# Optimization experiments

Hardware: AMD Instinct MI355X
Metric: run time of the kernel (lower is better)

## Reference

```python
import jax, jax.numpy as jnp
import numpy as np

INITIAL_CAPITAL = 500.0
TRANSACTION_COST = 0.0003
TAU = 1.0  # gumbel-softmax temperature
B, S, F = 256, 4096, 64


def setup_inputs() -> dict:
    key = jax.random.key(0)
    ks = jax.random.split(key, 10)
    features = jax.random.normal(ks[0], (B, S, F), dtype=jnp.float32)
    # make columns 1/2 look like vix level / vix change so branches fire
    features = features.at[:, :, 1].set(20.0 + 10.0 * jax.random.uniform(ks[1], (B, S)))
    features = features.at[:, :, 2].set(0.5 * jax.random.normal(ks[2], (B, S)))
    features = features.at[:, :, 3].set(0.01 * jax.random.normal(ks[3], (B, S)))
    return {
        "features": features,
        "feature_weights": jnp.ones((F,), jnp.float32) / F,
        "long_threshold": jnp.float32(0.52),
        "short_threshold": jnp.float32(0.48),
        "base_position_size": jnp.float32(0.8),
        "conviction_scalar": jnp.float32(0.5),
        "vix_impact": jnp.float32(0.2),
        "vix_collapse_threshold": jnp.float32(0.15),
        "vix_spike_threshold": jnp.float32(0.15),
        "gumbel_noise": jax.random.gumbel(ks[4], (S, B, 3), dtype=jnp.float32),
    }


def reference(features, feature_weights, long_threshold, short_threshold,
              base_position_size, conviction_scalar, vix_impact,
              vix_collapse_threshold, vix_spike_threshold, gumbel_noise):
    batch, seq_len, _ = features.shape
    # predictions: sigmoid of feature-weighted sum  [B,S]
    predictions = jax.nn.sigmoid(jnp.einsum('bsf,f->bs', features, feature_weights))
    # time-major per-step inputs [S,B]
    pred_t = predictions.T
    mom_t = features[:, :, 0].T
    vix_t = features[:, :, 1].T
    vch_t = features[:, :, 2].T
    mret_t = features[:, :, 3].T

    def step(carry, x):
        eq, pos = carry  # eq [B], pos [B,3]
        p, v, dv, m, r, g = x
        signal_strength = jnp.abs(p - 0.5) / 0.5
        vix_collapse = (dv < -vix_collapse_threshold) & (v < 30.0)
        vix_spike = (dv > vix_spike_threshold) & (v > 20.0)
        psz = jnp.clip(base_position_size + conviction_scalar * signal_strength, 0.2, 1.0)
        psz = jnp.where(vix_collapse | vix_spike, psz * (1.0 + vix_impact), psz)
        long_pos = ((p >= long_threshold) & (m > 0)) | vix_collapse
        short_pos = ((p <= short_threshold) & (m < 0)) | vix_spike
        logits = jnp.stack([
            jnp.where(long_pos, 1.0, -10.0),
            jnp.where(short_pos, 1.0, -10.0),
            jnp.where(~long_pos & ~short_pos, 1.0, -10.0),
        ], axis=1)  # [B,3]
        probs = jax.nn.softmax((logits + g) / TAU, axis=1)
        strategy_return = psz * (probs[:, 0] - probs[:, 1]) * r
        position_change = jnp.abs(probs - pos).sum(axis=1)
        eq_new = eq * (1.0 + strategy_return - position_change * TRANSACTION_COST)
        return (eq_new, probs), (eq_new, probs, psz)

    eq0 = jnp.full((batch,), INITIAL_CAPITAL, dtype=features.dtype)
    pos0 = jnp.zeros((batch, 3), features.dtype).at[:, 2].set(1.0)
    (_, _), (eq_seq, pos_seq, psz_seq) = jax.lax.scan(
        step, (eq0, pos0), (pred_t, vix_t, vch_t, mom_t, mret_t, gumbel_noise))
    equity = jnp.concatenate([eq0[:, None], eq_seq.T], axis=1)          # [B,S+1]
    positions = jnp.concatenate([pos0[:, None], jnp.swapaxes(pos_seq, 0, 1)], axis=1)  # [B,S+1,3]
    position_sizes = psz_seq[-1]  # last timestep, matching torch loop leak
    return equity, positions, predictions, position_sizes
```

## Files before the change

### kernel.cpp

```cpp
#include <hip/hip_runtime.h>

#define Bn 256
#define Sn 4096
#define Fn 64
#define TCOST 0.0003f
#define INIT_CAP 500.0f

#define EQ_OFF   0
#define POS_OFF  (Bn * (Sn + 1))
#define PRED_OFF (Bn * (Sn + 1) * 4)
#define PSZ_OFF  (PRED_OFF + Bn * Sn)

__global__ __launch_bounds__(256) void gumbel_transpose(
    const float* __restrict__ gin,
    float* __restrict__ gout)
{
    __shared__ float tile[32 * 97];
    int s0 = (blockIdx.x & 127) * 32;
    int b0 = (blockIdx.x >> 7) * 32;

    for (int idx = threadIdx.x; idx < 32 * 96; idx += 256) {
        int i = idx / 96;
        int rem = idx - i * 96;
        tile[i * 97 + rem] = gin[(size_t)(s0 + i) * (Bn * 3) + b0 * 3 + rem];
    }
    __syncthreads();
    for (int idx = threadIdx.x; idx < 32 * 96; idx += 256) {
        int j = idx / 96;
        int rem = idx - j * 96;
        int i = rem / 3;
        int c = rem - i * 3;
        gout[(size_t)(b0 + j) * (Sn * 3) + (size_t)(s0 + i) * 3 + c] =
            tile[i * 97 + j * 3 + c];
    }
}

__global__ __launch_bounds__(256) void trishot_fwd(
    const float* __restrict__ feat,
    const float* __restrict__ w,
    const float* __restrict__ p_lt, const float* __restrict__ p_st,
    const float* __restrict__ p_bps, const float* __restrict__ p_cs,
    const float* __restrict__ p_vi, const float* __restrict__ p_vct,
    const float* __restrict__ p_vst,
    const float* __restrict__ gt,
    float* __restrict__ out)
{
    __shared__ float xs[256];
    __shared__ float m0s[256], v0s[256], d0s[256], r0s[256];

    int t = threadIdx.x;
    int R0 = blockIdx.x * 256;
    int g = t >> 4;
    int l = t & 15;

    float4 wv = ((const float4*)w)[l];

#pragma unroll
    for (int q = 0; q < 16; q++) {
        int row = R0 + q * 16 + g;
        float4 fv = ((const float4*)feat)[(size_t)row * 16 + l];
        float partial = fmaf(fv.x, wv.x,
                        fmaf(fv.y, wv.y,
                        fmaf(fv.z, wv.z, fv.w * wv.w)));
        partial += __shfl_xor(partial, 1, 64);
        partial += __shfl_xor(partial, 2, 64);
        partial += __shfl_xor(partial, 4, 64);
        partial += __shfl_xor(partial, 8, 64);
        if (l == 0) {
            int rr = q * 16 + g;
            xs[rr]  = partial;
            m0s[rr] = fv.x;
            v0s[rr] = fv.y;
            d0s[rr] = fv.z;
            r0s[rr] = fv.w;
        }
    }
    __syncthreads();

    int r = R0 + t;
    int b = r >> 12;
    int s = r & (Sn - 1);

    const float LT = *p_lt, ST = *p_st, BPS = *p_bps, CS = *p_cs,
                VI = *p_vi, VCT = *p_vct, VST = *p_vst;

    float x = xs[t];
    float p = 1.0f / (1.0f + __expf(-x));
    float mom = m0s[t], vix = v0s[t], dvix = d0s[t], mret = r0s[t];

    float ss = fabsf(p - 0.5f) * 2.0f;
    bool collapse = (dvix < -VCT) && (vix < 30.0f);
    bool spike    = (dvix >  VST) && (vix > 20.0f);
    float psz = fminf(fmaxf(BPS + CS * ss, 0.2f), 1.0f);
    if (collapse || spike) psz *= (1.0f + VI);

    bool lp = ((p >= LT) && (mom > 0.0f)) || collapse;
    bool sp = ((p <= ST) && (mom < 0.0f)) || spike;
    float l0 = lp ? 1.0f : -10.0f;
    float l1 = sp ? 1.0f : -10.0f;
    float l2 = (!lp && !sp) ? 1.0f : -10.0f;

    const float* gg = gt + (size_t)r * 3;
    float g0 = gg[0], g1 = gg[1], g2 = gg[2];
    float z0 = l0 + g0, z1 = l1 + g1, z2 = l2 + g2;
    float zm = fmaxf(z0, fmaxf(z1, z2));
    float e0 = __expf(z0 - zm), e1 = __expf(z1 - zm), e2 = __expf(z2 - zm);
    float inv = 1.0f / (e0 + e1 + e2);
    float q0 = e0 * inv, q1 = e1 * inv, q2 = e2 * inv;

    out[PRED_OFF + r] = p;

    size_t prow = ((size_t)b * (Sn + 1) + s + 1) * 3;
    float* pos = out + POS_OFF;
    pos[prow + 0] = q0;
    pos[prow + 1] = q1;
    pos[prow + 2] = q2;

    out[EQ_OFF + (size_t)b * (Sn + 1) + s + 1] = psz * (q0 - q1) * mret;

    if (s == 0) {
        size_t p0row = (size_t)b * (Sn + 1) * 3;
        pos[p0row + 0] = 0.0f;
        pos[p0row + 1] = 0.0f;
        pos[p0row + 2] = 1.0f;
    }
    if (s == Sn - 1) {
        out[PSZ_OFF + b] = psz;
    }
}

#define CH 16
__global__ __launch_bounds__(256) void trishot_scan(float* __restrict__ out)
{
    int b = blockIdx.x;
    int j = threadIdx.x;

    float* eq = out + EQ_OFF + (size_t)b * (Sn + 1);
    const float* pos = out + POS_OFF + (size_t)b * (Sn + 1) * 3;

    int t0 = j * CH;
    float prev0 = pos[(size_t)t0 * 3 + 0];
    float prev1 = pos[(size_t)t0 * 3 + 1];
    float prev2 = pos[(size_t)t0 * 3 + 2];

    float f[CH];
    float lprod = 1.0f;
#pragma unroll
    for (int i = 0; i < CH; i++) {
        size_t ci = (size_t)(t0 + i + 1) * 3;
        float c0 = pos[ci + 0], c1 = pos[ci + 1], c2 = pos[ci + 2];
        float pc = fabsf(c0 - prev0) + fabsf(c1 - prev1) + fabsf(c2 - prev2);
        float rp = eq[t0 + i + 1];
        float fac = 1.0f + rp - pc * TCOST;
        f[i] = fac;
        lprod *= fac;
        prev0 = c0; prev1 = c1; prev2 = c2;
    }

    __shared__ float sc[256];
    sc[j] = lprod;
    __syncthreads();
#pragma unroll
    for (int off = 1; off < 256; off <<= 1) {
        float mine = sc[j];
        float other = (j >= off) ? sc[j - off] : 1.0f;
        __syncthreads();
        sc[j] = mine * other;
        __syncthreads();
    }

    float eqv = INIT_CAP * ((j > 0) ? sc[j - 1] : 1.0f);
#pragma unroll
    for (int i = 0; i < CH; i++) {
        eqv *= f[i];
        eq[t0 + i + 1] = eqv;
    }
    if (j == 0) eq[0] = INIT_CAP;
}

extern "C" void kernel_launch(void* const* d_in, const int* in_sizes, int n_in,
                              void* d_out, int out_size, void* d_ws, size_t ws_size,
                              hipStream_t stream) {
    const float* feat   = (const float*)d_in[0];
    const float* w      = (const float*)d_in[1];
    const float* lt     = (const float*)d_in[2];
    const float* st     = (const float*)d_in[3];
    const float* bps    = (const float*)d_in[4];
    const float* cs     = (const float*)d_in[5];
    const float* vi     = (const float*)d_in[6];
    const float* vct    = (const float*)d_in[7];
    const float* vst    = (const float*)d_in[8];
    const float* gumbel = (const float*)d_in[9];
    float* out = (float*)d_out;
    float* gt  = (float*)d_ws;

    gumbel_transpose<<<128 * 8, 256, 0, stream>>>(gumbel, gt);
    trishot_fwd<<<(Bn * Sn) / 256, 256, 0, stream>>>(
        feat, w, lt, st, bps, cs, vi, vct, vst, gt, out);
    trishot_scan<<<Bn, 256, 0, stream>>>(out);
}
```

Before: 402.1 us.

## Fuse forward pass and equity scan into one block-per-batch kernel

Merges the per-row forward kernel and the equity scan kernel into a single kernel with one 1024-thread block per batch row. Softmax positions and per-step factors stay in shared memory, so the scan no longer re-reads positions and returns from global memory, and one launch is dropped. In exchange, grid parallelism falls to one block per batch, shared memory use grows, and chunked processing adds block-wide barriers, which can reduce latency hiding for the large feature read.

After: 396.6 us. About the same (-1.4%).

```diff
diff --git a/kernel.cpp b/kernel.cpp
--- a/kernel.cpp
+++ b/kernel.cpp
@@ -35,7 +35,7 @@
     }
 }
 
-__global__ __launch_bounds__(256) void trishot_fwd(
+__global__ __launch_bounds__(1024) void trishot_fused(
     const float* __restrict__ feat,
     const float* __restrict__ w,
     const float* __restrict__ p_lt, const float* __restrict__ p_st,
@@ -45,137 +45,123 @@
     const float* __restrict__ gt,
     float* __restrict__ out)
 {
-    __shared__ float xs[256];
-    __shared__ float m0s[256], v0s[256], d0s[256], r0s[256];
+    __shared__ float qL[(Sn + 1) * 3];
+    __shared__ float facL[Sn];
+    __shared__ float xs[1024];
+    __shared__ float m0s[1024], v0s[1024], d0s[1024], r0s[1024];
+    __shared__ float scanL[1024];
 
+    int b = blockIdx.x;
     int t = threadIdx.x;
-    int R0 = blockIdx.x * 256;
     int g = t >> 4;
     int l = t & 15;
-
-    float4 wv = ((const float4*)w)[l];
-
-#pragma unroll
-    for (int q = 0; q < 16; q++) {
-        int row = R0 + q * 16 + g;
-        float4 fv = ((const float4*)feat)[(size_t)row * 16 + l];
-        float partial = fmaf(fv.x, wv.x,
-                        fmaf(fv.y, wv.y,
-                        fmaf(fv.z, wv.z, fv.w * wv.w)));
-        partial += __shfl_xor(partial, 1, 64);
-        partial += __shfl_xor(partial, 2, 64);
-        partial += __shfl_xor(partial, 4, 64);
-        partial += __shfl_xor(partial, 8, 64);
-        if (l == 0) {
-            int rr = q * 16 + g;
-            xs[rr]  = partial;
-            m0s[rr] = fv.x;
-            v0s[rr] = fv.y;
-            d0s[rr] = fv.z;
-            r0s[rr] = fv.w;
-        }
-    }
-    __syncthreads();
-
-    int r = R0 + t;
-    int b = r >> 12;
-    int s = r & (Sn - 1);
 
     const float LT = *p_lt, ST = *p_st, BPS = *p_bps, CS = *p_cs,
                 VI = *p_vi, VCT = *p_vct, VST = *p_vst;
 
-    float x = xs[t];
-    float p = 1.0f / (1.0f + __expf(-x));
-    float mom = m0s[t], vix = v0s[t], dvix = d0s[t], mret = r0s[t];
+    float4 wv = ((const float4*)w)[l];
 
-    float ss = fabsf(p - 0.5f) * 2.0f;
-    bool collapse = (dvix < -VCT) && (vix < 30.0f);
-    bool spike    = (dvix >  VST) && (vix > 20.0f);
-    float psz = fminf(fmaxf(BPS + CS * ss, 0.2f), 1.0f);
-    if (collapse || spike) psz *= (1.0f + VI);
+    if (t == 0) { qL[0] = 0.0f; qL[1] = 0.0f; qL[2] = 1.0f; }
 
-    bool lp = ((p >= LT) && (mom > 0.0f)) || collapse;
-    bool sp = ((p <= ST) && (mom < 0.0f)) || spike;
-    float l0 = lp ? 1.0f : -10.0f;
-    float l1 = sp ? 1.0f : -10.0f;
-    float l2 = (!lp && !sp) ? 1.0f : -10.0f;
+    float* pos = out + POS_OFF;
 
-    const float* gg = gt + (size_t)r * 3;
-    float g0 = gg[0], g1 = gg[1], g2 = gg[2];
-    float z0 = l0 + g0, z1 = l1 + g1, z2 = l2 + g2;
-    float zm = fmaxf(z0, fmaxf(z1, z2));
-    float e0 = __expf(z0 - zm), e1 = __expf(z1 - zm), e2 = __expf(z2 - zm);
-    float inv = 1.0f / (e0 + e1 + e2);
-    float q0 = e0 * inv, q1 = e1 * inv, q2 = e2 * inv;
+    for (int c = 0; c < 4; c++) {
+#pragma unroll
+        for (int q = 0; q < 16; q++) {
+            int i = q * 64 + g;
+            size_t row = (size_t)b * Sn + c * 1024 + i;
+            float4 fv = ((const float4*)feat)[row * 16 + l];
+            float partial = fmaf(fv.x, wv.x,
+                            fmaf(fv.y, wv.y,
+                            fmaf(fv.z, wv.z, fv.w * wv.w)));
+            partial += __shfl_xor(partial, 1, 64);
+            partial += __shfl_xor(partial, 2, 64);
+            partial += __shfl_xor(partial, 4, 64);
+            partial += __shfl_xor(partial, 8, 64);
+            if (l == 0) {
+                xs[i]  = partial;
+                m0s[i] = fv.x;
+                v0s[i] = fv.y;
+                d0s[i] = fv.z;
+                r0s[i] = fv.w;
+            }
+        }
+        __syncthreads();
 
-    out[PRED_OFF + r] = p;
+        int s = c * 1024 + t;
+        float x = xs[t];
+        float p = 1.0f / (1.0f + __expf(-x));
+        float mom = m0s[t], vix = v0s[t], dvix = d0s[t], mret = r0s[t];
 
-    size_t prow = ((size_t)b * (Sn + 1) + s + 1) * 3;
-    float* pos = out + POS_OFF;
-    pos[prow + 0] = q0;
-    pos[prow + 1] = q1;
-    pos[prow + 2] = q2;
+        float ss = fabsf(p - 0.5f) * 2.0f;
+        bool collapse = (dvix < -VCT) && (vix < 30.0f);
+        bool spike    = (dvix >  VST) && (vix > 20.0f);
+        float psz = fminf(fmaxf(BPS + CS * ss, 0.2f), 1.0f);
+        if (collapse || spike) psz *= (1.0f + VI);
 
-    out[EQ_OFF + (size_t)b * (Sn + 1) + s + 1] = psz * (q0 - q1) * mret;
+        bool lp = ((p >= LT) && (mom > 0.0f)) || collapse;
+        bool sp = ((p <= ST) && (mom < 0.0f)) || spike;
+        float l0 = lp ? 1.0f : -10.0f;
+        float l1 = sp ? 1.0f : -10.0f;
+        float l2 = (!lp && !sp) ? 1.0f : -10.0f;
 
-    if (s == 0) {
+        const float* gg = gt + ((size_t)b * Sn + s) * 3;
+        float z0 = l0 + gg[0], z1 = l1 + gg[1], z2 = l2 + gg[2];
+        float zm = fmaxf(z0, fmaxf(z1, z2));
+        float e0 = __expf(z0 - zm), e1 = __expf(z1 - zm), e2 = __expf(z2 - zm);
+        float inv = 1.0f / (e0 + e1 + e2);
+        float q0 = e0 * inv, q1 = e1 * inv, q2 = e2 * inv;
+
+        qL[(s + 1) * 3 + 0] = q0;
+        qL[(s + 1) * 3 + 1] = q1;
+        qL[(s + 1) * 3 + 2] = q2;
+
+        out[PRED_OFF + (size_t)b * Sn + s] = p;
+        size_t prow = ((size_t)b * (Sn + 1) + s + 1) * 3;
+        pos[prow + 0] = q0;
+        pos[prow + 1] = q1;
+        pos[prow + 2] = q2;
+        if (s == Sn - 1) out[PSZ_OFF + b] = psz;
+
+        float rp = psz * (q0 - q1) * mret;
+        __syncthreads();
+
+        float pm0 = qL[s * 3 + 0], pm1 = qL[s * 3 + 1], pm2 = qL[s * 3 + 2];
+        float pc = fabsf(q0 - pm0) + fabsf(q1 - pm1) + fabsf(q2 - pm2);
+        facL[s] = 1.0f + rp - pc * TCOST;
+        __syncthreads();
+    }
+
+    float f0 = facL[4 * t + 0];
+    float f1 = facL[4 * t + 1];
+    float f2 = facL[4 * t + 2];
+    float f3 = facL[4 * t + 3];
+    float lprod = ((f0 * f1) * (f2 * f3));
+    scanL[t] = lprod;
+    __syncthreads();
+#pragma unroll
+    for (int off = 1; off < 1024; off <<= 1) {
+        float mine = scanL[t];
+        float other = (t >= off) ? scanL[t - off] : 1.0f;
+        __syncthreads();
+        scanL[t] = mine * other;
+        __syncthreads();
+    }
+
+    float* eq = out + EQ_OFF + (size_t)b * (Sn + 1);
+    float eqv = INIT_CAP * ((t > 0) ? scanL[t - 1] : 1.0f);
+    eqv *= f0; eq[4 * t + 1] = eqv;
+    eqv *= f1; eq[4 * t + 2] = eqv;
+    eqv *= f2; eq[4 * t + 3] = eqv;
+    eqv *= f3; eq[4 * t + 4] = eqv;
+
+    if (t == 0) {
+        eq[0] = INIT_CAP;
         size_t p0row = (size_t)b * (Sn + 1) * 3;
         pos[p0row + 0] = 0.0f;
         pos[p0row + 1] = 0.0f;
         pos[p0row + 2] = 1.0f;
     }
-    if (s == Sn - 1) {
-        out[PSZ_OFF + b] = psz;
-    }
-}
-
-#define CH 16
-__global__ __launch_bounds__(256) void trishot_scan(float* __restrict__ out)
-{
-    int b = blockIdx.x;
-    int j = threadIdx.x;
-
-    float* eq = out + EQ_OFF + (size_t)b * (Sn + 1);
-    const float* pos = out + POS_OFF + (size_t)b * (Sn + 1) * 3;
-
-    int t0 = j * CH;
-    float prev0 = pos[(size_t)t0 * 3 + 0];
-    float prev1 = pos[(size_t)t0 * 3 + 1];
-    float prev2 = pos[(size_t)t0 * 3 + 2];
-
-    float f[CH];
-    float lprod = 1.0f;
-#pragma unroll
-    for (int i = 0; i < CH; i++) {
-        size_t ci = (size_t)(t0 + i + 1) * 3;
-        float c0 = pos[ci + 0], c1 = pos[ci + 1], c2 = pos[ci + 2];
-        float pc = fabsf(c0 - prev0) + fabsf(c1 - prev1) + fabsf(c2 - prev2);
-        float rp = eq[t0 + i + 1];
-        float fac = 1.0f + rp - pc * TCOST;
-        f[i] = fac;
-        lprod *= fac;
-        prev0 = c0; prev1 = c1; prev2 = c2;
-    }
-
-    __shared__ float sc[256];
-    sc[j] = lprod;
-    __syncthreads();
-#pragma unroll
-    for (int off = 1; off < 256; off <<= 1) {
-        float mine = sc[j];
-        float other = (j >= off) ? sc[j - off] : 1.0f;
-        __syncthreads();
-        sc[j] = mine * other;
-        __syncthreads();
-    }
-
-    float eqv = INIT_CAP * ((j > 0) ? sc[j - 1] : 1.0f);
-#pragma unroll
-    for (int i = 0; i < CH; i++) {
-        eqv *= f[i];
-        eq[t0 + i + 1] = eqv;
-    }
-    if (j == 0) eq[0] = INIT_CAP;
 }
 
 extern "C" void kernel_launch(void* const* d_in, const int* in_sizes, int n_in,
@@ -195,7 +181,6 @@
     float* gt  = (float*)d_ws;
 
     gumbel_transpose<<<128 * 8, 256, 0, stream>>>(gumbel, gt);
-    trishot_fwd<<<(Bn * Sn) / 256, 256, 0, stream>>>(
+    trishot_fused<<<Bn, 1024, 0, stream>>>(
         feat, w, lt, st, bps, cs, vi, vct, vst, gt, out);
-    trishot_scan<<<Bn, 256, 0, stream>>>(out);
 }
```

## Compute per-step equity factor in forward kernel, drop position reads in scan

Applied to the files above, without the earlier changes.

The forward kernel now keeps each block's softmax probabilities in shared memory and also computes the previous row's probabilities for the block boundary. With those it computes the full per-step growth factor (1 + return - transaction cost) directly. The scan kernel then reads only that factor and no longer re-reads the positions array from global memory. This removes about 3 floats per step of global reads in the scan, at the cost of a small redundant boundary-row computation and an extra barrier per block.

After: 402.6 us. Within noise of the previous version (+0.1%).

```diff
diff --git a/kernel.cpp b/kernel.cpp
--- a/kernel.cpp
+++ b/kernel.cpp
@@ -47,13 +47,52 @@
 {
     __shared__ float xs[256];
     __shared__ float m0s[256], v0s[256], d0s[256], r0s[256];
+    __shared__ float qs[257 * 3];
 
     int t = threadIdx.x;
     int R0 = blockIdx.x * 256;
     int g = t >> 4;
     int l = t & 15;
 
+    const float LT = *p_lt, ST = *p_st, BPS = *p_bps, CS = *p_cs,
+                VI = *p_vi, VCT = *p_vct, VST = *p_vst;
+
     float4 wv = ((const float4*)w)[l];
+
+    int s0 = R0 & (Sn - 1);
+    int b = R0 >> 12;
+
+    if (t < 16) {
+        if (s0 == 0) {
+            if (t == 0) { qs[0] = 0.0f; qs[1] = 0.0f; qs[2] = 1.0f; }
+        } else {
+            float4 fv = ((const float4*)feat)[(size_t)(R0 - 1) * 16 + t];
+            float partial = fmaf(fv.x, wv.x,
+                            fmaf(fv.y, wv.y,
+                            fmaf(fv.z, wv.z, fv.w * wv.w)));
+            partial += __shfl_xor(partial, 1, 64);
+            partial += __shfl_xor(partial, 2, 64);
+            partial += __shfl_xor(partial, 4, 64);
+            partial += __shfl_xor(partial, 8, 64);
+            if (t == 0) {
+                float p = 1.0f / (1.0f + __expf(-partial));
+                float mom = fv.x, vix = fv.y, dvix = fv.z;
+                bool collapse = (dvix < -VCT) && (vix < 30.0f);
+                bool spike    = (dvix >  VST) && (vix > 20.0f);
+                bool lp = ((p >= LT) && (mom > 0.0f)) || collapse;
+                bool sp = ((p <= ST) && (mom < 0.0f)) || spike;
+                float l0 = lp ? 1.0f : -10.0f;
+                float l1 = sp ? 1.0f : -10.0f;
+                float l2 = (!lp && !sp) ? 1.0f : -10.0f;
+                const float* gg = gt + (size_t)(R0 - 1) * 3;
+                float z0 = l0 + gg[0], z1 = l1 + gg[1], z2 = l2 + gg[2];
+                float zm = fmaxf(z0, fmaxf(z1, z2));
+                float e0 = __expf(z0 - zm), e1 = __expf(z1 - zm), e2 = __expf(z2 - zm);
+                float inv = 1.0f / (e0 + e1 + e2);
+                qs[0] = e0 * inv; qs[1] = e1 * inv; qs[2] = e2 * inv;
+            }
+        }
+    }
 
 #pragma unroll
     for (int q = 0; q < 16; q++) {
@@ -77,13 +116,7 @@
     }
     __syncthreads();
 
-    int r = R0 + t;
-    int b = r >> 12;
-    int s = r & (Sn - 1);
-
-    const float LT = *p_lt, ST = *p_st, BPS = *p_bps, CS = *p_cs,
-                VI = *p_vi, VCT = *p_vct, VST = *p_vst;
-
+    int s = s0 + t;
     float x = xs[t];
     float p = 1.0f / (1.0f + __expf(-x));
     float mom = m0s[t], vix = v0s[t], dvix = d0s[t], mret = r0s[t];
@@ -100,33 +133,37 @@
     float l1 = sp ? 1.0f : -10.0f;
     float l2 = (!lp && !sp) ? 1.0f : -10.0f;
 
-    const float* gg = gt + (size_t)r * 3;
-    float g0 = gg[0], g1 = gg[1], g2 = gg[2];
-    float z0 = l0 + g0, z1 = l1 + g1, z2 = l2 + g2;
+    const float* gg = gt + (size_t)(R0 + t) * 3;
+    float z0 = l0 + gg[0], z1 = l1 + gg[1], z2 = l2 + gg[2];
     float zm = fmaxf(z0, fmaxf(z1, z2));
     float e0 = __expf(z0 - zm), e1 = __expf(z1 - zm), e2 = __expf(z2 - zm);
     float inv = 1.0f / (e0 + e1 + e2);
     float q0 = e0 * inv, q1 = e1 * inv, q2 = e2 * inv;
 
-    out[PRED_OFF + r] = p;
-
+    qs[(t + 1) * 3 + 0] = q0;
+    qs[(t + 1) * 3 + 1] = q1;
+    qs[(t + 1) * 3 + 2] = q2;
+
+    out[PRED_OFF + R0 + t] = p;
+    float* pos = out + POS_OFF;
     size_t prow = ((size_t)b * (Sn + 1) + s + 1) * 3;
-    float* pos = out + POS_OFF;
     pos[prow + 0] = q0;
     pos[prow + 1] = q1;
     pos[prow + 2] = q2;
-
-    out[EQ_OFF + (size_t)b * (Sn + 1) + s + 1] = psz * (q0 - q1) * mret;
-
+    if (s == Sn - 1) out[PSZ_OFF + b] = psz;
     if (s == 0) {
         size_t p0row = (size_t)b * (Sn + 1) * 3;
         pos[p0row + 0] = 0.0f;
         pos[p0row + 1] = 0.0f;
         pos[p0row + 2] = 1.0f;
     }
-    if (s == Sn - 1) {
-        out[PSZ_OFF + b] = psz;
-    }
+
+    float rp = psz * (q0 - q1) * mret;
+    __syncthreads();
+
+    float pm0 = qs[t * 3 + 0], pm1 = qs[t * 3 + 1], pm2 = qs[t * 3 + 2];
+    float pc = fabsf(q0 - pm0) + fabsf(q1 - pm1) + fabsf(q2 - pm2);
+    out[EQ_OFF + (size_t)b * (Sn + 1) + s + 1] = 1.0f + rp - pc * TCOST;
 }
 
 #define CH 16
@@ -134,27 +171,16 @@
 {
     int b = blockIdx.x;
     int j = threadIdx.x;
-
     float* eq = out + EQ_OFF + (size_t)b * (Sn + 1);
-    const float* pos = out + POS_OFF + (size_t)b * (Sn + 1) * 3;
 
     int t0 = j * CH;
-    float prev0 = pos[(size_t)t0 * 3 + 0];
-    float prev1 = pos[(size_t)t0 * 3 + 1];
-    float prev2 = pos[(size_t)t0 * 3 + 2];
-
     float f[CH];
     float lprod = 1.0f;
 #pragma unroll
     for (int i = 0; i < CH; i++) {
-        size_t ci = (size_t)(t0 + i + 1) * 3;
-        float c0 = pos[ci + 0], c1 = pos[ci + 1], c2 = pos[ci + 2];
-        float pc = fabsf(c0 - prev0) + fabsf(c1 - prev1) + fabsf(c2 - prev2);
-        float rp = eq[t0 + i + 1];
-        float fac = 1.0f + rp - pc * TCOST;
+        float fac = eq[t0 + i + 1];
         f[i] = fac;
         lprod *= fac;
-        prev0 = c0; prev1 = c1; prev2 = c2;
     }
 
     __shared__ float sc[256];
```
